# Optimization experiments

Measured on AMD Instinct MI355X. Metric: run time of the kernel, lower is better.

Reference implementation:

```python
import jax, jax.numpy as jnp
import numpy as np
from jax import lax

D_MODEL = 384
D_INNER = 768   # expand * d_model
D_STATE = 16
DT_RANK = 24
K_CONV = 4
B_SZ = 2
L_SEQ = 2048


def setup_inputs() -> dict:
    key = jax.random.key(0)
    ks = jax.random.split(key, 11)
    inp = {}
    inp["x"] = jax.random.normal(ks[0], (B_SZ, L_SEQ, D_MODEL), dtype=jnp.float32)
    # learned parameters (Mamba block)
    inp["in_proj_w"] = jax.random.normal(ks[1], (D_MODEL, 2 * D_INNER), dtype=jnp.float32) * 0.02
    inp["conv_w"] = jax.random.normal(ks[2], (D_INNER, K_CONV), dtype=jnp.float32) * 0.1
    inp["conv_b"] = jnp.zeros((D_INNER,), dtype=jnp.float32)
    inp["x_proj_w"] = jax.random.normal(ks[3], (D_INNER, DT_RANK + 2 * D_STATE), dtype=jnp.float32) * 0.02
    inp["dt_proj_w"] = jax.random.normal(ks[4], (DT_RANK, D_INNER), dtype=jnp.float32) * 0.1
    inp["dt_proj_b"] = jnp.full((D_INNER,), -2.0, dtype=jnp.float32)  # softplus(-2) ~ small init dt
    # A_log initialized so A = -exp(A_log) = -[1..d_state]
    inp["A_log"] = jnp.log(jnp.broadcast_to(jnp.arange(1, D_STATE + 1, dtype=jnp.float32), (D_INNER, D_STATE)))
    inp["D"] = jnp.ones((D_INNER,), dtype=jnp.float32)
    inp["out_proj_w"] = jax.random.normal(ks[5], (D_INNER, D_MODEL), dtype=jnp.float32) * 0.02
    return inp


def _silu(x):
    return x * jax.nn.sigmoid(x)


def reference(x, in_proj_w, conv_w, conv_b, x_proj_w, dt_proj_w, dt_proj_b, A_log, D, out_proj_w):
    B, L, _ = x.shape
    d_inner, n = A_log.shape
    k = conv_w.shape[-1]

    # input projection and gate split
    xz = jnp.einsum("bld,de->ble", x, in_proj_w)          # [B, L, 2*d_inner]
    xp, z = jnp.split(xz, 2, axis=-1)                       # each [B, L, d_inner]

    # causal depthwise 1D conv along sequence
    xp_t = xp.transpose(0, 2, 1)                            # [B, d_inner, L]
    conv_out = lax.conv_general_dilated(
        xp_t, conv_w[:, None, :],                           # kernel [O=d_inner, I/g=1, K]
        window_strides=(1,), padding=[(k - 1, 0)],
        dimension_numbers=("NCH", "OIH", "NCH"),
        feature_group_count=d_inner,
    ) + conv_b[None, :, None]
    xp = _silu(conv_out.transpose(0, 2, 1))                 # [B, L, d_inner]

    # data-dependent SSM parameters
    x_dbl = jnp.einsum("bld,de->ble", xp, x_proj_w)         # [B, L, dt_rank + 2n]
    dt_r = x_dbl[..., :DT_RANK]
    Bm = x_dbl[..., DT_RANK:DT_RANK + n]                    # [B, L, n]
    Cm = x_dbl[..., DT_RANK + n:]                           # [B, L, n]
    dt = jax.nn.softplus(jnp.einsum("blr,rd->bld", dt_r, dt_proj_w) + dt_proj_b)  # [B, L, d_inner]

    A = -jnp.exp(A_log)                                     # [d_inner, n]
    dA = jnp.exp(jnp.einsum("bld,dn->bldn", dt, A))         # discretized state transition
    dBx = jnp.einsum("bln,bld->bldn", Bm, dt * xp)          # input contribution

    # sequential selective scan over L
    def step(h, inputs):
        dA_t, dBx_t, C_t = inputs                           # [B,d,n],[B,d,n],[B,n]
        h = dA_t * h + dBx_t
        y = jnp.einsum("bdn,bn->bd", h, C_t)
        return h, y

    h0 = jnp.zeros((B, d_inner, n), dtype=x.dtype)
    _, ys = lax.scan(step, h0, (dA.transpose(1, 0, 2, 3), dBx.transpose(1, 0, 2, 3), Cm.transpose(1, 0, 2)))
    y = ys.transpose(1, 0, 2)                               # [B, L, d_inner]

    y = y + xp * D                                          # skip term
    y = y * _silu(z)                                        # gating
    return jnp.einsum("bld,de->ble", y, out_proj_w)         # [B, L, d_model]
```

## Files before the change

### kernel.cpp

```cpp
#include <hip/hip_runtime.h>
#include <hip/hip_bf16.h>

#define B_SZ    2
#define L_SEQ   2048
#define D_MODEL 384
#define D_INNER 768
#define D_STATE 16
#define DT_RANK 24
#define ML      (B_SZ * L_SEQ)
#define NCHUNK  64
#define CHLEN   (L_SEQ / NCHUNK)

typedef __hip_bfloat16 bf16;
typedef __attribute__((ext_vector_type(8))) short bf16x8;
typedef __attribute__((ext_vector_type(4))) float f32x4;
typedef __attribute__((ext_vector_type(8))) float f32x8;

template<int EPI, int AMODE>
__global__ __launch_bounds__(256)
void gemm_mfma(const float* __restrict__ Af, const bf16* __restrict__ At,
               const float* __restrict__ W,
               bf16* __restrict__ outb0, bf16* __restrict__ outb1,
               float* __restrict__ outf, int M, int N, int K)
{
    __shared__ __attribute__((aligned(16))) short As[64][72];
    __shared__ __attribute__((aligned(16))) short Bs[64][72];
    const int tid  = threadIdx.x;
    const int lane = tid & 63;
    const int wave = tid >> 6;
    const int wm   = (wave & 1) * 32;
    const int wn   = (wave >> 1) * 32;
    const int m0   = blockIdx.y * 64;
    const int n0   = blockIdx.x * 64;

    f32x4 acc[2][2];
#pragma unroll
    for (int i = 0; i < 2; i++)
#pragma unroll
        for (int j = 0; j < 2; j++)
#pragma unroll
            for (int r = 0; r < 4; r++) acc[i][j][r] = 0.f;

    for (int kt = 0; kt < K; kt += 64) {
        __syncthreads();
#pragma unroll
        for (int i = 0; i < 2; i++) {
            int c = tid + 256 * i;
            if (AMODE == 0) {
                int m = c >> 3, k8 = (c & 7) * 8;
                f32x8 a = *(const f32x8*)&Af[(size_t)(m0 + m) * K + kt + k8];
                bf16x8 h;
#pragma unroll
                for (int j = 0; j < 8; j++)
                    h[j] = (short)__bfloat16_as_ushort(__float2bfloat16(a[j]));
                *(bf16x8*)&As[m][k8] = h;
            } else {
                int m8 = (c & 7) * 8, k = c >> 3;
                bf16x8 a = *(const bf16x8*)&At[(size_t)(kt + k) * M + m0 + m8];
#pragma unroll
                for (int j = 0; j < 8; j++) As[m8 + j][k] = a[j];
            }
        }
#pragma unroll
        for (int i = 0; i < 2; i++) {
            int c = tid + 256 * i;
            int n8 = (c & 7) * 8, k = c >> 3;
            if (n0 + n8 + 8 <= N) {
                f32x8 w = *(const f32x8*)&W[(size_t)(kt + k) * N + n0 + n8];
#pragma unroll
                for (int j = 0; j < 8; j++)
                    Bs[n8 + j][k] = (short)__bfloat16_as_ushort(__float2bfloat16(w[j]));
            } else {
#pragma unroll
                for (int j = 0; j < 8; j++) Bs[n8 + j][k] = 0;
            }
        }
        __syncthreads();
#pragma unroll
        for (int ks = 0; ks < 2; ks++) {
            int kb = ks * 32 + (lane >> 4) * 8;
            bf16x8 a0 = *(const bf16x8*)&As[wm + (lane & 15)][kb];
            bf16x8 a1 = *(const bf16x8*)&As[wm + 16 + (lane & 15)][kb];
            bf16x8 b0 = *(const bf16x8*)&Bs[wn + (lane & 15)][kb];
            bf16x8 b1 = *(const bf16x8*)&Bs[wn + 16 + (lane & 15)][kb];
            acc[0][0] = __builtin_amdgcn_mfma_f32_16x16x32_bf16(a0, b0, acc[0][0], 0, 0, 0);
            acc[0][1] = __builtin_amdgcn_mfma_f32_16x16x32_bf16(a0, b1, acc[0][1], 0, 0, 0);
            acc[1][0] = __builtin_amdgcn_mfma_f32_16x16x32_bf16(a1, b0, acc[1][0], 0, 0, 0);
            acc[1][1] = __builtin_amdgcn_mfma_f32_16x16x32_bf16(a1, b1, acc[1][1], 0, 0, 0);
        }
    }

#pragma unroll
    for (int am = 0; am < 2; am++)
#pragma unroll
        for (int bn = 0; bn < 2; bn++)
#pragma unroll
            for (int r = 0; r < 4; r++) {
                int m = m0 + wm + am * 16 + (lane >> 4) * 4 + r;
                int n = n0 + wn + bn * 16 + (lane & 15);
                float v = acc[am][bn][r];
                if (EPI == 0) {
                    if (n < D_INNER)
                        outb0[(size_t)n * ML + m] = __float2bfloat16(v);
                    else
                        outb1[(size_t)(n - D_INNER) * ML + m] =
                            __float2bfloat16(v / (1.f + __expf(-v)));
                } else {
                    if (n < N) outf[(size_t)m * N + n] = v;
                }
            }
}

__global__ __launch_bounds__(256)
void gemm_xproj_split(const bf16* __restrict__ At, const float* __restrict__ W,
                      float* __restrict__ outf, int M, int N, int K)
{
    __shared__ __attribute__((aligned(16))) short As[64][72];
    __shared__ __attribute__((aligned(16))) short Bs[64][72];
    const int tid  = threadIdx.x;
    const int lane = tid & 63;
    const int wave = tid >> 6;
    const int wm   = (wave & 1) * 32;
    const int wn   = (wave >> 1) * 32;
    const int m0   = blockIdx.y * 64;
    const int k0   = blockIdx.x * (768 / 4);

    f32x4 acc[2][2];
#pragma unroll
    for (int i = 0; i < 2; i++)
#pragma unroll
        for (int j = 0; j < 2; j++)
#pragma unroll
            for (int r = 0; r < 4; r++) acc[i][j][r] = 0.f;

    for (int kt = k0; kt < k0 + 192; kt += 64) {
        __syncthreads();
#pragma unroll
        for (int i = 0; i < 2; i++) {
            int c = tid + 256 * i;
            int m8 = (c & 7) * 8, k = c >> 3;
            bf16x8 a = *(const bf16x8*)&At[(size_t)(kt + k) * M + m0 + m8];
#pragma unroll
            for (int j = 0; j < 8; j++) As[m8 + j][k] = a[j];
        }
#pragma unroll
        for (int i = 0; i < 2; i++) {
            int c = tid + 256 * i;
            int n8 = (c & 7) * 8, k = c >> 3;
            if (n8 + 8 <= N) {
                f32x8 w = *(const f32x8*)&W[(size_t)(kt + k) * N + n8];
#pragma unroll
                for (int j = 0; j < 8; j++)
                    Bs[n8 + j][k] = (short)__bfloat16_as_ushort(__float2bfloat16(w[j]));
            } else {
#pragma unroll
                for (int j = 0; j < 8; j++) Bs[n8 + j][k] = 0;
            }
        }
        __syncthreads();
#pragma unroll
        for (int ks = 0; ks < 2; ks++) {
            int kb = ks * 32 + (lane >> 4) * 8;
            bf16x8 a0 = *(const bf16x8*)&As[wm + (lane & 15)][kb];
            bf16x8 a1 = *(const bf16x8*)&As[wm + 16 + (lane & 15)][kb];
            bf16x8 b0 = *(const bf16x8*)&Bs[wn + (lane & 15)][kb];
            bf16x8 b1 = *(const bf16x8*)&Bs[wn + 16 + (lane & 15)][kb];
            acc[0][0] = __builtin_amdgcn_mfma_f32_16x16x32_bf16(a0, b0, acc[0][0], 0, 0, 0);
            acc[0][1] = __builtin_amdgcn_mfma_f32_16x16x32_bf16(a0, b1, acc[0][1], 0, 0, 0);
            acc[1][0] = __builtin_amdgcn_mfma_f32_16x16x32_bf16(a1, b0, acc[1][0], 0, 0, 0);
            acc[1][1] = __builtin_amdgcn_mfma_f32_16x16x32_bf16(a1, b1, acc[1][1], 0, 0, 0);
        }
    }

#pragma unroll
    for (int am = 0; am < 2; am++)
#pragma unroll
        for (int bn = 0; bn < 2; bn++)
#pragma unroll
            for (int r = 0; r < 4; r++) {
                int m = m0 + wm + am * 16 + (lane >> 4) * 4 + r;
                int n = wn + bn * 16 + (lane & 15);
                if (n < N)
                    atomicAdd(&outf[(size_t)m * N + n], acc[am][bn][r]);
            }
}

__global__ __launch_bounds__(256)
void gemm_outproj_split(const bf16* __restrict__ At, const float* __restrict__ W,
                        float* __restrict__ outf)
{
    __shared__ __attribute__((aligned(16))) short As[64][72];
    __shared__ __attribute__((aligned(16))) short Bs[64][72];
    const int tid  = threadIdx.x;
    const int lane = tid & 63;
    const int wave = tid >> 6;
    const int wm   = (wave & 1) * 32;
    const int wn   = (wave >> 1) * 32;
    const int n0   = blockIdx.x * 64;
    const int m0   = blockIdx.y * 64;
    const int k0   = blockIdx.z * (768 / 4);

    f32x4 acc[2][2];
#pragma unroll
    for (int i = 0; i < 2; i++)
#pragma unroll
        for (int j = 0; j < 2; j++)
#pragma unroll
            for (int r = 0; r < 4; r++) acc[i][j][r] = 0.f;

    for (int kt = k0; kt < k0 + 192; kt += 64) {
        __syncthreads();
#pragma unroll
        for (int i = 0; i < 2; i++) {
            int c = tid + 256 * i;
            int m8 = (c & 7) * 8, k = c >> 3;
            bf16x8 a = *(const bf16x8*)&At[(size_t)(kt + k) * ML + m0 + m8];
#pragma unroll
            for (int j = 0; j < 8; j++) As[m8 + j][k] = a[j];
        }
#pragma unroll
        for (int i = 0; i < 2; i++) {
            int c = tid + 256 * i;
            int n8 = (c & 7) * 8, k = c >> 3;
            f32x8 w = *(const f32x8*)&W[(size_t)(kt + k) * D_MODEL + n0 + n8];
#pragma unroll
            for (int j = 0; j < 8; j++)
                Bs[n8 + j][k] = (short)__bfloat16_as_ushort(__float2bfloat16(w[j]));
        }
        __syncthreads();
#pragma unroll
        for (int ks = 0; ks < 2; ks++) {
            int kb = ks * 32 + (lane >> 4) * 8;
            bf16x8 a0 = *(const bf16x8*)&As[wm + (lane & 15)][kb];
            bf16x8 a1 = *(const bf16x8*)&As[wm + 16 + (lane & 15)][kb];
            bf16x8 b0 = *(const bf16x8*)&Bs[wn + (lane & 15)][kb];
            bf16x8 b1 = *(const bf16x8*)&Bs[wn + 16 + (lane & 15)][kb];
            acc[0][0] = __builtin_amdgcn_mfma_f32_16x16x32_bf16(a0, b0, acc[0][0], 0, 0, 0);
            acc[0][1] = __builtin_amdgcn_mfma_f32_16x16x32_bf16(a0, b1, acc[0][1], 0, 0, 0);
            acc[1][0] = __builtin_amdgcn_mfma_f32_16x16x32_bf16(a1, b0, acc[1][0], 0, 0, 0);
            acc[1][1] = __builtin_amdgcn_mfma_f32_16x16x32_bf16(a1, b1, acc[1][1], 0, 0, 0);
        }
    }

#pragma unroll
    for (int am = 0; am < 2; am++)
#pragma unroll
        for (int bn = 0; bn < 2; bn++)
#pragma unroll
            for (int r = 0; r < 4; r++) {
                int m = m0 + wm + am * 16 + (lane >> 4) * 4 + r;
                int n = n0 + wn + bn * 16 + (lane & 15);
                atomicAdd(&outf[(size_t)m * D_MODEL + n], acc[am][bn][r]);
            }
}

__global__ __launch_bounds__(256)
void conv_silu_kernel(const bf16* __restrict__ xp_raw_t,
                      const float* __restrict__ cw, const float* __restrict__ cb,
                      bf16* __restrict__ xp_t, float* __restrict__ x_dbl_zero,
                      float* __restrict__ out_zero)
{
    {
        int gidx = (blockIdx.y * gridDim.x + blockIdx.x) * 256 + threadIdx.x;
        if (gidx < ML * 56) x_dbl_zero[gidx] = 0.f;
        f32x4 z;
        z[0] = 0.f; z[1] = 0.f; z[2] = 0.f; z[3] = 0.f;
        *(f32x4*)&out_zero[(size_t)gidx * 4] = z;
    }

    const int ml0 = (blockIdx.x * 256 + threadIdx.x) * 8;
    const int d   = blockIdx.y;
    const int l0  = ml0 & (L_SEQ - 1);
    const size_t row = (size_t)d * ML;
    const float w0 = cw[d * 4 + 0], w1 = cw[d * 4 + 1],
                w2 = cw[d * 4 + 2], w3 = cw[d * 4 + 3], bias = cb[d];

    bf16x8 cur = *(const bf16x8*)&xp_raw_t[row + ml0];
    bf16x8 prev;
    if (ml0 != 0) prev = *(const bf16x8*)&xp_raw_t[row + ml0 - 8];
    else {
#pragma unroll
        for (int j = 0; j < 8; j++) prev[j] = 0;
    }
    float w[16];
#pragma unroll
    for (int k = 0; k < 8; k++) {
        w[k]     = __uint_as_float(((unsigned)(unsigned short)prev[k]) << 16);
        w[k + 8] = __uint_as_float(((unsigned)(unsigned short)cur[k]) << 16);
    }

    bf16x8 out;
#pragma unroll
    for (int o = 0; o < 8; o++) {
        int l = l0 + o;
        float s = bias;
        if (l >= 3) {
            s += w0 * w[5 + o] + w1 * w[6 + o] + w2 * w[7 + o] + w3 * w[8 + o];
        } else {
            if (l - 3 >= 0) s += w0 * w[5 + o];
            if (l - 2 >= 0) s += w1 * w[6 + o];
            if (l - 1 >= 0) s += w2 * w[7 + o];
            s += w3 * w[8 + o];
        }
        float act = s / (1.f + __expf(-s));
        out[o] = (short)__bfloat16_as_ushort(__float2bfloat16(act));
    }
    *(bf16x8*)&xp_t[row + ml0] = out;
}

__global__ __launch_bounds__(256)
void dt_kernel(const float* __restrict__ x_dbl, const float* __restrict__ dtw,
               const float* __restrict__ dtb, bf16* __restrict__ dt_t)
{
    __shared__ float xs[64 * 25];
    __shared__ float ws[24 * 48];
    const int tid = threadIdx.x;
    const int m0 = blockIdx.x * 64;
    const int d0 = blockIdx.y * 48;
#pragma unroll
    for (int i = 0; i < 6; i++) {
        int idx = tid + 256 * i;
        int r_ = idx / 24, cc = idx % 24;
        xs[r_ * 25 + cc] = x_dbl[(size_t)(m0 + r_) * 56 + cc];
    }
#pragma unroll
    for (int i = 0; i < 5; i++) {
        int idx = tid + 256 * i;
        if (idx < 24 * 48) {
            int r_ = idx / 48, dd = idx % 48;
            ws[idx] = dtw[r_ * D_INNER + d0 + dd];
        }
    }
    __syncthreads();
#pragma unroll
    for (int i = 0; i < 12; i++) {
        int o = tid + 256 * i;
        int mloc = o & 63, dd = o >> 6;
        float acc = dtb[d0 + dd];
#pragma unroll
        for (int r_ = 0; r_ < 24; r_++)
            acc += xs[mloc * 25 + r_] * ws[r_ * 48 + dd];
        float sp = fmaxf(acc, 0.f) + log1pf(__expf(-fabsf(acc)));
        dt_t[(size_t)(d0 + dd) * ML + m0 + mloc] = __float2bfloat16(sp);
    }
}

__global__ __launch_bounds__(1024)
void scan_kernel(const bf16* __restrict__ dt_t, const bf16* __restrict__ xp_t,
                 const float* __restrict__ x_dbl, const bf16* __restrict__ zs_t,
                 const float* __restrict__ A_log, const float* __restrict__ Dp,
                 bf16* __restrict__ y_t)
{
    __shared__ float sP[NCHUNK][D_STATE + 1];
    __shared__ float sH[NCHUNK][D_STATE + 1];
    const int tid = threadIdx.x;
    const int c = tid >> 4;
    const int n = tid & 15;
    const int g = blockIdx.x;
    const int b = g / D_INNER;
    const int d = g % D_INNER;
    const float A = -__expf(A_log[d * D_STATE + n]);
    const size_t base_t = (size_t)d * ML + (size_t)b * L_SEQ + (size_t)c * CHLEN;
    const size_t base_m = (size_t)b * L_SEQ + (size_t)c * CHLEN;

    float h = 0.f, P = 1.f;
#pragma unroll
    for (int g2 = 0; g2 < 2; g2++) {
        bf16x8 vdt0 = *(const bf16x8*)&dt_t[base_t + g2 * 16];
        bf16x8 vdt1 = *(const bf16x8*)&dt_t[base_t + g2 * 16 + 8];
        bf16x8 vxp0 = *(const bf16x8*)&xp_t[base_t + g2 * 16];
        bf16x8 vxp1 = *(const bf16x8*)&xp_t[base_t + g2 * 16 + 8];
#pragma unroll
        for (int k = 0; k < 16; k++) {
            const int j = g2 * 16 + k;
            short sdt = (k < 8) ? vdt0[k & 7] : vdt1[k & 7];
            short sxp = (k < 8) ? vxp0[k & 7] : vxp1[k & 7];
            float dtv = __uint_as_float(((unsigned)(unsigned short)sdt) << 16);
            float xpv = __uint_as_float(((unsigned)(unsigned short)sxp) << 16);
            float Bn  = x_dbl[(base_m + j) * 56 + DT_RANK + n];
            float aj = __expf(dtv * A);
            h = aj * h + Bn * (dtv * xpv);
            P *= aj;
        }
    }
    sP[c][n] = P;
    sH[c][n] = h;
    __syncthreads();

    {
        const int wv = tid >> 6;
        const int ln = tid & 63;
        float p = sP[ln][wv];
        float hh = sH[ln][wv];
#pragma unroll
        for (int s = 1; s < NCHUNK; s <<= 1) {
            float p2 = __shfl_up(p, s);
            float h2 = __shfl_up(hh, s);
            if (ln >= s) { hh = p * h2 + hh; p = p * p2; }
        }
        sP[ln][wv] = p;
        sH[ln][wv] = hh;
    }
    __syncthreads();
    const float hinit = (c == 0) ? 0.f : sH[c - 1][n];

    const float Dd = Dp[d];
    h = hinit;
#pragma unroll
    for (int g2 = 0; g2 < 2; g2++) {
        bf16x8 vdt0 = *(const bf16x8*)&dt_t[base_t + g2 * 16];
        bf16x8 vdt1 = *(const bf16x8*)&dt_t[base_t + g2 * 16 + 8];
        bf16x8 vxp0 = *(const bf16x8*)&xp_t[base_t + g2 * 16];
        bf16x8 vxp1 = *(const bf16x8*)&xp_t[base_t + g2 * 16 + 8];
        float ymine = 0.f, xmine = 0.f;
#pragma unroll
        for (int k = 0; k < 16; k++) {
            const int j = g2 * 16 + k;
            short sdt = (k < 8) ? vdt0[k & 7] : vdt1[k & 7];
            short sxp = (k < 8) ? vxp0[k & 7] : vxp1[k & 7];
            float dtv = __uint_as_float(((unsigned)(unsigned short)sdt) << 16);
            float xpv = __uint_as_float(((unsigned)(unsigned short)sxp) << 16);
            float Bn  = x_dbl[(base_m + j) * 56 + DT_RANK + n];
            float aj = __expf(dtv * A);
            h = aj * h + Bn * (dtv * xpv);
            float Cn = x_dbl[(base_m + j) * 56 + DT_RANK + D_STATE + n];
            float yv = h * Cn;
            yv += __shfl_xor(yv, 1);
            yv += __shfl_xor(yv, 2);
            yv += __shfl_xor(yv, 4);
            yv += __shfl_xor(yv, 8);
            ymine = (k == n) ? yv : ymine;
            xmine = (k == n) ? xpv : xmine;
        }
        const int j = g2 * 16 + n;
        float zsv = __bfloat162float(zs_t[base_t + j]);
        y_t[base_t + j] = __float2bfloat16((ymine + xmine * Dd) * zsv);
    }
}

extern "C" void kernel_launch(void* const* d_in, const int* in_sizes, int n_in,
                              void* d_out, int out_size, void* d_ws, size_t ws_size,
                              hipStream_t stream)
{
    const float* x         = (const float*)d_in[0];
    const float* in_proj_w = (const float*)d_in[1];
    const float* conv_w    = (const float*)d_in[2];
    const float* conv_b    = (const float*)d_in[3];
    const float* x_proj_w  = (const float*)d_in[4];
    const float* dt_proj_w = (const float*)d_in[5];
    const float* dt_proj_b = (const float*)d_in[6];
    const float* A_log     = (const float*)d_in[7];
    const float* Dvec      = (const float*)d_in[8];
    const float* out_proj_w= (const float*)d_in[9];

    bf16* xp_raw_t = (bf16*)d_ws;
    bf16* zs_t     = xp_raw_t + (size_t)ML * D_INNER;
    bf16* xp_t     = zs_t     + (size_t)ML * D_INNER;
    bf16* dt_t     = xp_t     + (size_t)ML * D_INNER;
    float* x_dbl   = (float*)(dt_t + (size_t)ML * D_INNER);
    bf16* y_t      = xp_raw_t;

    dim3 blk(256);

    gemm_mfma<0, 0><<<dim3(2 * D_INNER / 64, ML / 64), blk, 0, stream>>>(
        x, nullptr, in_proj_w, xp_raw_t, zs_t, nullptr, ML, 2 * D_INNER, D_MODEL);

    conv_silu_kernel<<<dim3(ML / 2048, D_INNER), blk, 0, stream>>>(
        xp_raw_t, conv_w, conv_b, xp_t, x_dbl, (float*)d_out);

    gemm_xproj_split<<<dim3(4, ML / 64), blk, 0, stream>>>(
        xp_t, x_proj_w, x_dbl, ML, 56, D_INNER);

    dt_kernel<<<dim3(ML / 64, D_INNER / 48), blk, 0, stream>>>(
        x_dbl, dt_proj_w, dt_proj_b, dt_t);

    scan_kernel<<<B_SZ * D_INNER, 1024, 0, stream>>>(
        dt_t, xp_t, x_dbl, zs_t, A_log, Dvec, y_t);

    gemm_outproj_split<<<dim3(D_MODEL / 64, ML / 64, 4), blk, 0, stream>>>(
        y_t, out_proj_w, (float*)d_out);
}
```

Measured before the change: 240.2 us.

## Fold dt projection into x_proj GEMM via precomputed combined weight

Precomputes a combined weight Wc = x_proj_w[:, :24] @ dt_proj_w (768x768) inside the conv kernel, then runs a single GEMM producing B/C columns and the dt columns with softplus in the epilogue. This removes the separate dt kernel, the split-K atomics and the x_dbl zeroing. In exchange the x_proj GEMM grows from 56 to 800 output columns, the dt path loses rank-24 precision through bf16 rounding of the combined weight, and the weight product is recomputed on every call.

```diff
diff --git a/kernel.cpp b/kernel.cpp
--- a/kernel.cpp
+++ b/kernel.cpp
@@ -10,6 +10,7 @@
 #define ML      (B_SZ * L_SEQ)
 #define NCHUNK  64
 #define CHLEN   (L_SEQ / NCHUNK)
+#define NPRJ    800
 
 typedef __hip_bfloat16 bf16;
 typedef __attribute__((ext_vector_type(8))) short bf16x8;
@@ -112,8 +113,9 @@
 }
 
 __global__ __launch_bounds__(256)
-void gemm_xproj_split(const bf16* __restrict__ At, const float* __restrict__ W,
-                      float* __restrict__ outf, int M, int N, int K)
+void gemm_xproj_dt(const bf16* __restrict__ At, const float* __restrict__ Wbc,
+                   const float* __restrict__ Wc, const float* __restrict__ dtb,
+                   float* __restrict__ x_dbl, bf16* __restrict__ dt_t)
 {
     __shared__ __attribute__((aligned(16))) short As[64][72];
     __shared__ __attribute__((aligned(16))) short Bs[64][72];
@@ -123,7 +125,7 @@
     const int wm   = (wave & 1) * 32;
     const int wn   = (wave >> 1) * 32;
     const int m0   = blockIdx.y * 64;
-    const int k0   = blockIdx.x * (768 / 4);
+    const int n0   = blockIdx.x * 64;
 
     f32x4 acc[2][2];
 #pragma unroll
@@ -133,13 +135,13 @@
 #pragma unroll
             for (int r = 0; r < 4; r++) acc[i][j][r] = 0.f;
 
-    for (int kt = k0; kt < k0 + 192; kt += 64) {
+    for (int kt = 0; kt < D_INNER; kt += 64) {
         __syncthreads();
 #pragma unroll
         for (int i = 0; i < 2; i++) {
             int c = tid + 256 * i;
             int m8 = (c & 7) * 8, k = c >> 3;
-            bf16x8 a = *(const bf16x8*)&At[(size_t)(kt + k) * M + m0 + m8];
+            bf16x8 a = *(const bf16x8*)&At[(size_t)(kt + k) * ML + m0 + m8];
 #pragma unroll
             for (int j = 0; j < 8; j++) As[m8 + j][k] = a[j];
         }
@@ -147,8 +149,14 @@
         for (int i = 0; i < 2; i++) {
             int c = tid + 256 * i;
             int n8 = (c & 7) * 8, k = c >> 3;
-            if (n8 + 8 <= N) {
-                f32x8 w = *(const f32x8*)&W[(size_t)(kt + k) * N + n8];
+            int gn = n0 + n8;
+            if (gn < 32) {
+                f32x8 w = *(const f32x8*)&Wbc[(size_t)(kt + k) * 56 + DT_RANK + gn];
+#pragma unroll
+                for (int j = 0; j < 8; j++)
+                    Bs[n8 + j][k] = (short)__bfloat16_as_ushort(__float2bfloat16(w[j]));
+            } else if (gn < NPRJ) {
+                f32x8 w = *(const f32x8*)&Wc[(size_t)(kt + k) * D_INNER + gn - 32];
 #pragma unroll
                 for (int j = 0; j < 8; j++)
                     Bs[n8 + j][k] = (short)__bfloat16_as_ushort(__float2bfloat16(w[j]));
@@ -179,9 +187,15 @@
 #pragma unroll
             for (int r = 0; r < 4; r++) {
                 int m = m0 + wm + am * 16 + (lane >> 4) * 4 + r;
-                int n = wn + bn * 16 + (lane & 15);
-                if (n < N)
-                    atomicAdd(&outf[(size_t)m * N + n], acc[am][bn][r]);
+                int n = n0 + wn + bn * 16 + (lane & 15);
+                float v = acc[am][bn][r];
+                if (n < 32) {
+                    x_dbl[(size_t)m * 56 + DT_RANK + n] = v;
+                } else if (n < NPRJ) {
+                    float a = v + dtb[n - 32];
+                    float sp = fmaxf(a, 0.f) + log1pf(__expf(-fabsf(a)));
+                    dt_t[(size_t)(n - 32) * ML + m] = __float2bfloat16(sp);
+                }
             }
 }
 
@@ -257,15 +271,27 @@
 __global__ __launch_bounds__(256)
 void conv_silu_kernel(const bf16* __restrict__ xp_raw_t,
                       const float* __restrict__ cw, const float* __restrict__ cb,
-                      bf16* __restrict__ xp_t, float* __restrict__ x_dbl_zero,
+                      const float* __restrict__ xpw, const float* __restrict__ dtw,
+                      bf16* __restrict__ xp_t, float* __restrict__ Wc,
                       float* __restrict__ out_zero)
 {
     {
         int gidx = (blockIdx.y * gridDim.x + blockIdx.x) * 256 + threadIdx.x;
-        if (gidx < ML * 56) x_dbl_zero[gidx] = 0.f;
         f32x4 z;
         z[0] = 0.f; z[1] = 0.f; z[2] = 0.f; z[3] = 0.f;
         *(f32x4*)&out_zero[(size_t)gidx * 4] = z;
+#pragma unroll
+        for (int t = 0; t < 2; t++) {
+            int e = gidx + t * 393216;
+            if (e < D_INNER * D_INNER) {
+                int k = e / D_INNER, d = e - k * D_INNER;
+                float s = 0.f;
+#pragma unroll
+                for (int r = 0; r < DT_RANK; r++)
+                    s += xpw[(size_t)k * 56 + r] * dtw[(size_t)r * D_INNER + d];
+                Wc[e] = s;
+            }
+        }
     }
 
     const int ml0 = (blockIdx.x * 256 + threadIdx.x) * 8;
@@ -306,43 +332,6 @@
         out[o] = (short)__bfloat16_as_ushort(__float2bfloat16(act));
     }
     *(bf16x8*)&xp_t[row + ml0] = out;
-}
-
-__global__ __launch_bounds__(256)
-void dt_kernel(const float* __restrict__ x_dbl, const float* __restrict__ dtw,
-               const float* __restrict__ dtb, bf16* __restrict__ dt_t)
-{
-    __shared__ float xs[64 * 25];
-    __shared__ float ws[24 * 48];
-    const int tid = threadIdx.x;
-    const int m0 = blockIdx.x * 64;
-    const int d0 = blockIdx.y * 48;
-#pragma unroll
-    for (int i = 0; i < 6; i++) {
-        int idx = tid + 256 * i;
-        int r_ = idx / 24, cc = idx % 24;
-        xs[r_ * 25 + cc] = x_dbl[(size_t)(m0 + r_) * 56 + cc];
-    }
-#pragma unroll
-    for (int i = 0; i < 5; i++) {
-        int idx = tid + 256 * i;
-        if (idx < 24 * 48) {
-            int r_ = idx / 48, dd = idx % 48;
-            ws[idx] = dtw[r_ * D_INNER + d0 + dd];
-        }
-    }
-    __syncthreads();
-#pragma unroll
-    for (int i = 0; i < 12; i++) {
-        int o = tid + 256 * i;
-        int mloc = o & 63, dd = o >> 6;
-        float acc = dtb[d0 + dd];
-#pragma unroll
-        for (int r_ = 0; r_ < 24; r_++)
-            acc += xs[mloc * 25 + r_] * ws[r_ * 48 + dd];
-        float sp = fmaxf(acc, 0.f) + log1pf(__expf(-fabsf(acc)));
-        dt_t[(size_t)(d0 + dd) * ML + m0 + mloc] = __float2bfloat16(sp);
-    }
 }
 
 __global__ __launch_bounds__(1024)
@@ -458,6 +447,7 @@
     bf16* xp_t     = zs_t     + (size_t)ML * D_INNER;
     bf16* dt_t     = xp_t     + (size_t)ML * D_INNER;
     float* x_dbl   = (float*)(dt_t + (size_t)ML * D_INNER);
+    float* Wc      = x_dbl + (size_t)ML * 56;
     bf16* y_t      = xp_raw_t;
 
     dim3 blk(256);
@@ -466,13 +456,10 @@
         x, nullptr, in_proj_w, xp_raw_t, zs_t, nullptr, ML, 2 * D_INNER, D_MODEL);
 
     conv_silu_kernel<<<dim3(ML / 2048, D_INNER), blk, 0, stream>>>(
-        xp_raw_t, conv_w, conv_b, xp_t, x_dbl, (float*)d_out);
-
-    gemm_xproj_split<<<dim3(4, ML / 64), blk, 0, stream>>>(
-        xp_t, x_proj_w, x_dbl, ML, 56, D_INNER);
-
-    dt_kernel<<<dim3(ML / 64, D_INNER / 48), blk, 0, stream>>>(
-        x_dbl, dt_proj_w, dt_proj_b, dt_t);
+        xp_raw_t, conv_w, conv_b, x_proj_w, dt_proj_w, xp_t, Wc, (float*)d_out);
+
+    gemm_xproj_dt<<<dim3((NPRJ + 63) / 64, ML / 64), blk, 0, stream>>>(
+        xp_t, x_proj_w, Wc, dt_proj_b, x_dbl, dt_t);
 
     scan_kernel<<<B_SZ * D_INNER, 1024, 0, stream>>>(
         dt_t, xp_t, x_dbl, zs_t, A_log, Dvec, y_t);
```

After: 276.5 us. +15.1%, slower.
